# Performance work log

Measured on AMD Instinct MI355X. Metric: run time of the kernel, lower is better.

The kernel has to match this reference:

```python
import jax, jax.numpy as jnp
import numpy as np

B, N = 64, 196
D1, D2, H = 512, 2048, 512


def setup_inputs() -> dict:
    key = jax.random.key(0)
    ks = jax.random.split(key, 8)
    s1 = 1.0 / np.sqrt(D1)
    s2 = 1.0 / np.sqrt(D2)
    sh = 1.0 / np.sqrt(H)
    return {
        "input1": jax.random.normal(ks[0], (B, D1), jnp.float32),
        "input2": jax.random.normal(ks[1], (B, N, D2), jnp.float32),
        "W1": jax.random.uniform(ks[2], (D1, H), jnp.float32, -s1, s1),
        "b1": jax.random.uniform(ks[3], (H,), jnp.float32, -s1, s1),
        "W2": jax.random.uniform(ks[4], (D2, H), jnp.float32, -s2, s2),
        "b2": jax.random.uniform(ks[5], (H,), jnp.float32, -s2, s2),
        "Wf": jax.random.uniform(ks[6], (H, 1), jnp.float32, -sh, sh),
        "bf": jax.random.uniform(ks[7], (1,), jnp.float32, -sh, sh),
    }


def reference(input1, input2, W1, b1, W2, b2, Wf, bf):
    # enc1: [B, H]; enc2: [B, N, H]
    enc1 = input1 @ W1 + b1
    enc2 = jnp.einsum("bnd,dh->bnh", input2, W2) + b2
    # additive (Bahdanau) score: relu(enc2 + enc1[:,None]) @ Wf -> [B, N]
    scores = (jax.nn.relu(enc2 + enc1[:, None, :]) @ Wf)[..., 0] + bf[0]
    alpha = jax.nn.softmax(scores, axis=1)  # softmax over N regions
    att = jnp.einsum("bnd,bn->bd", input2, alpha)  # weighted sum of raw features
    return att, alpha
```

## Files before the change

kernel.cpp:

```cpp
#include <hip/hip_runtime.h>
#include <hip/hip_bf16.h>
#include <stdint.h>

#define BB 64
#define NN 196
#define D1c 512
#define D2c 2048
#define HHc 512
#define MM (BB*NN)

typedef __attribute__((ext_vector_type(8))) short bf16x8;
typedef __attribute__((ext_vector_type(4))) float f32x4;

__device__ inline ushort f2bf(float f){
  uint32_t u = __float_as_uint(f);
  u += 0x7fff + ((u >> 16) & 1);
  return (ushort)(u >> 16);
}
__device__ inline uint32_t cvtpk(float lo, float hi){
  uint32_t r;
  asm("v_cvt_pk_bf16_f32 %0, %1, %2" : "=v"(r) : "v"(lo), "v"(hi));
  return r;
}

__global__ __launch_bounds__(256) void w2t_kernel(const float* __restrict__ W2,
                                                  ushort* __restrict__ w2t){
  __shared__ float tile[64][65];
  const int kt = blockIdx.x;
  const int ht = blockIdx.y;
  const int t = threadIdx.x;
  const int tr = t >> 4;
  const int tc = (t & 15) * 4;
  #pragma unroll
  for (int p = 0; p < 4; ++p){
    int k = p*16 + tr;
    float4 v = *(const float4*)(W2 + (size_t)(kt*64 + k)*HHc + ht*64 + tc);
    tile[k][tc] = v.x; tile[k][tc+1] = v.y; tile[k][tc+2] = v.z; tile[k][tc+3] = v.w;
  }
  __syncthreads();
  #pragma unroll
  for (int p = 0; p < 4; ++p){
    int h = p*16 + tr;
    ushort4 o;
    o.x = f2bf(tile[tc  ][h]);
    o.y = f2bf(tile[tc+1][h]);
    o.z = f2bf(tile[tc+2][h]);
    o.w = f2bf(tile[tc+3][h]);
    *(ushort4*)(w2t + (size_t)(ht*64 + h)*D2c + kt*64 + tc) = o;
  }
}

__global__ __launch_bounds__(128) void enc1_kernel(const float* __restrict__ in1,
                                                   const float* __restrict__ W1,
                                                   const float* __restrict__ b1,
                                                   float* __restrict__ enc1){
  __shared__ float s1[D1c];
  const int b = blockIdx.x;
  const int ht = blockIdx.y;
  const int t = threadIdx.x;
  ((float4*)s1)[t] = ((const float4*)(in1 + (size_t)b*D1c))[t];
  __syncthreads();
  const int h = ht*128 + t;
  float acc = b1[h];
  #pragma unroll 8
  for (int d = 0; d < D1c; ++d)
    acc += s1[d] * W1[(size_t)d*HHc + h];
  enc1[b*HHc + h] = acc;
}

__global__ __launch_bounds__(512,2) void score_gemm(
    const float*  __restrict__ in2,
    const ushort* __restrict__ w2t,
    const float*  __restrict__ b2,
    const float*  __restrict__ wf,
    const float*  __restrict__ enc1,
    float*        __restrict__ scores)
{
  __shared__ ushort As[2][128*64];
  __shared__ ushort Bs[3][256*64];

  const int t = threadIdx.x;
  const int p   = blockIdx.x;
  const int xcd = p & 7;
  const int lg  = (xcd < 4 ? xcd*25 : 100 + (xcd-4)*24) + (p >> 3);
  const int h0  = (lg & 1) * 256;
  const int m0  = (lg >> 1) * 128;

  const int wave = t >> 6, lane = t & 63;
  const int wm = wave >> 2, whh = wave & 3;
  const int l15 = lane & 15, l4 = lane >> 4;

  const int rA = wave*16 + l4;
  const float* aBase = in2 + (size_t)(m0 + rA)*D2c + l15*4;
  const int acw  = l15 >> 1;
  const int apar = (l15 & 1) * 4;

  const int bl_r = lane >> 3;
  const int bl_c = (lane & 7) ^ bl_r;

  f32x4 acc[4][4];
  #pragma unroll
  for (int i = 0; i < 4; ++i)
    #pragma unroll
    for (int j = 0; j < 4; ++j) acc[i][j] = (f32x4)0.f;

  float4 aReg[4];

#define A_LOAD(kt)                                                           \
  { _Pragma("unroll")                                                        \
    for (int j = 0; j < 4; ++j)                                              \
      aReg[j] = *(const float4*)(aBase + (size_t)(j*4)*D2c + (kt)*64); }

#define A_WRITE(buf)                                                         \
  { _Pragma("unroll")                                                        \
    for (int j = 0; j < 4; ++j){                                             \
      int r = rA + j*4;                                                      \
      uint2 pk;                                                              \
      pk.x = cvtpk(aReg[j].x, aReg[j].y);                                    \
      pk.y = cvtpk(aReg[j].z, aReg[j].w);                                    \
      *(uint2*)(As[buf] + r*64 + ((acw ^ (r & 7)) << 3) + apar) = pk; } }

#define B_GLDS(kt, buf)                                                      \
  { _Pragma("unroll")                                                        \
    for (int i = 0; i < 4; ++i){                                             \
      int g = wave*4 + i;                                                    \
      const ushort* src = w2t + (size_t)(h0 + g*8 + bl_r)*D2c                \
                          + (kt)*64 + bl_c*8;                                \
      __builtin_amdgcn_global_load_lds(                                      \
          (const __attribute__((address_space(1))) uint32_t*)src,            \
          (__attribute__((address_space(3))) uint32_t*)(Bs[buf] + g*512),    \
          16, 0, 0); } }

#define COMPUTE(abuf, bbuf)                                                  \
  { _Pragma("unroll")                                                        \
    for (int kk = 0; kk < 2; ++kk){                                          \
      bf16x8 af[4], bfr[4];                                                  \
      _Pragma("unroll")                                                      \
      for (int mf = 0; mf < 4; ++mf){                                        \
        int r = wm*64 + mf*16 + l15, c = kk*4 + l4;                          \
        af[mf] = *(const bf16x8*)(As[abuf] + r*64 + ((c ^ (r & 7)) << 3)); } \
      _Pragma("unroll")                                                      \
      for (int hf = 0; hf < 4; ++hf){                                        \
        int r = whh*64 + hf*16 + l15, c = kk*4 + l4;                         \
        bfr[hf] = *(const bf16x8*)(Bs[bbuf] + r*64 + ((c ^ (r & 7)) << 3)); }\
      _Pragma("unroll")                                                      \
      for (int mf = 0; mf < 4; ++mf)                                         \
        _Pragma("unroll")                                                    \
        for (int hf = 0; hf < 4; ++hf)                                       \
          acc[mf][hf] = __builtin_amdgcn_mfma_f32_16x16x32_bf16(             \
              af[mf], bfr[hf], acc[mf][hf], 0, 0, 0); } }

#define SB0()    __builtin_amdgcn_sched_barrier(0)
#define WAITV(n) { asm volatile("s_waitcnt vmcnt(" #n ")" ::: "memory"); SB0(); }
#define LGKM0()  { asm volatile("s_waitcnt lgkmcnt(0)" ::: "memory"); SB0(); }
#define BAR()    { SB0(); __builtin_amdgcn_s_barrier(); SB0(); }

  A_LOAD(0);
  B_GLDS(0, 0);
  B_GLDS(1, 1);
  SB0();
  WAITV(8);
  A_WRITE(0);
  WAITV(4);
  LGKM0();
  BAR();

  #pragma unroll 1
  for (int kt = 0; kt < 30; ++kt){
    A_LOAD(kt + 1);
    B_GLDS(kt + 2, (kt + 2) % 3);
    SB0();
    COMPUTE(kt & 1, kt % 3);
    WAITV(4);
    A_WRITE((kt + 1) & 1);
    LGKM0();
    BAR();
  }
  A_LOAD(31);
  SB0();
  COMPUTE(0, 0);
  WAITV(0);
  A_WRITE(1);
  LGKM0();
  BAR();
  COMPUTE(1, 1);

  float b2v[4], wfv[4];
  #pragma unroll
  for (int hf = 0; hf < 4; ++hf){
    int hc = h0 + whh*64 + hf*16 + l15;
    b2v[hf] = b2[hc]; wfv[hf] = wf[hc];
  }
  #pragma unroll
  for (int mf = 0; mf < 4; ++mf){
    #pragma unroll
    for (int r = 0; r < 4; ++r){
      int m = m0 + wm*64 + mf*16 + l4*4 + r;
      int b = m / NN;
      const float* e1 = enc1 + (size_t)b*HHc + h0 + whh*64 + l15;
      float s = 0.f;
      #pragma unroll
      for (int hf = 0; hf < 4; ++hf){
        float v = acc[mf][hf][r] + b2v[hf] + e1[hf*16];
        s += fmaxf(v, 0.f) * wfv[hf];
      }
      s += __shfl_xor(s, 1); s += __shfl_xor(s, 2);
      s += __shfl_xor(s, 4); s += __shfl_xor(s, 8);
      if (l15 == 0) atomicAdd(&scores[m], s);
    }
  }
#undef A_LOAD
#undef A_WRITE
#undef B_GLDS
#undef COMPUTE
#undef WAITV
#undef LGKM0
#undef SB0
#undef BAR
}

__global__ __launch_bounds__(64) void softmax_kernel(const float* __restrict__ scores,
                                                     float* __restrict__ alpha){
  const int b = blockIdx.x, t = threadIdx.x;
  const float* s = scores + b*NN;
  float x[4]; float mx = -1e30f;
  #pragma unroll
  for (int i = 0; i < 4; ++i){
    int n = t + i*64;
    x[i] = (n < NN) ? s[n] : -1e30f;
    mx = fmaxf(mx, x[i]);
  }
  #pragma unroll
  for (int o = 1; o < 64; o <<= 1) mx = fmaxf(mx, __shfl_xor(mx, o));
  float sum = 0.f;
  #pragma unroll
  for (int i = 0; i < 4; ++i){
    int n = t + i*64;
    float e = (n < NN) ? __expf(x[i] - mx) : 0.f;
    x[i] = e; sum += e;
  }
  #pragma unroll
  for (int o = 1; o < 64; o <<= 1) sum += __shfl_xor(sum, o);
  float inv = 1.f / sum;
  #pragma unroll
  for (int i = 0; i < 4; ++i){
    int n = t + i*64;
    if (n < NN) alpha[b*NN + n] = x[i] * inv;
  }
}

__global__ __launch_bounds__(256) void att_kernel(const float* __restrict__ in2,
                                                  const float* __restrict__ alpha,
                                                  float* __restrict__ att){
  __shared__ float sal[NN];
  const int b = blockIdx.y;
  const int t = threadIdx.x;
  if (t < NN) sal[t] = alpha[b*NN + t];
  __syncthreads();
  const int d = blockIdx.x*256 + t;
  const float* src = in2 + (size_t)b*NN*D2c + d;
  float acc = 0.f;
  #pragma unroll 7
  for (int n = 0; n < NN; ++n)
    acc += src[(size_t)n*D2c] * sal[n];
  att[(size_t)b*D2c + d] = acc;
}

extern "C" void kernel_launch(void* const* d_in, const int* in_sizes, int n_in,
                              void* d_out, int out_size, void* d_ws, size_t ws_size,
                              hipStream_t stream){
  (void)in_sizes; (void)n_in; (void)out_size; (void)ws_size;
  const float* input1 = (const float*)d_in[0];
  const float* input2 = (const float*)d_in[1];
  const float* W1     = (const float*)d_in[2];
  const float* b1     = (const float*)d_in[3];
  const float* W2     = (const float*)d_in[4];
  const float* b2     = (const float*)d_in[5];
  const float* Wf     = (const float*)d_in[6];

  float* out   = (float*)d_out;
  float* att   = out;
  float* alpha = out + BB*D2c;

  char*   ws     = (char*)d_ws;
  ushort* w2t    = (ushort*)ws;
  float*  enc1   = (float*)(ws + 2*1024*1024);
  float*  scores = (float*)(ws + 2*1024*1024 + 131072);

  hipMemsetAsync(scores, 0, MM*sizeof(float), stream);
  w2t_kernel<<<dim3(32, 8), 256, 0, stream>>>(W2, w2t);
  enc1_kernel<<<dim3(BB, 4), 128, 0, stream>>>(input1, W1, b1, enc1);
  score_gemm<<<dim3(196), 512, 0, stream>>>(input2, w2t, b2, Wf, enc1, scores);
  softmax_kernel<<<dim3(BB), 64, 0, stream>>>(scores, alpha);
  att_kernel<<<dim3(8, BB), 256, 0, stream>>>(input2, alpha, att);
}
```

Before: 109.6 us.

## Double-buffer A register prefetch and interleave fragment reads with MFMA in GEMM loop

The fp32 A-tile global loads are now issued two k-steps ahead into alternating register sets, which gives them a full iteration of latency hiding. Both k-halves' LDS fragments are read up front, and partial lgkmcnt waits let the first MFMA batch start while later reads are still in flight. MFMA sections are wrapped in s_setprio to favour matrix issue. The cost is more registers (two A register sets, two fragment sets), which could lower occupancy or cause spills.

New measurement: 118.3 us. 1.08x slower.

```diff
diff --git a/kernel.cpp b/kernel.cpp
--- a/kernel.cpp
+++ b/kernel.cpp
@@ -104,20 +104,21 @@
     #pragma unroll
     for (int j = 0; j < 4; ++j) acc[i][j] = (f32x4)0.f;
 
-  float4 aReg[4];
-
-#define A_LOAD(kt)                                                           \
+  float4 aRegA[4], aRegB[4];
+  bf16x8 af0[4], bf0[4], af1[4], bf1[4];
+
+#define A_LOAD(kt, R)                                                        \
   { _Pragma("unroll")                                                        \
     for (int j = 0; j < 4; ++j)                                              \
-      aReg[j] = *(const float4*)(aBase + (size_t)(j*4)*D2c + (kt)*64); }
-
-#define A_WRITE(buf)                                                         \
+      R[j] = *(const float4*)(aBase + (size_t)(j*4)*D2c + (kt)*64); }
+
+#define A_WRITE(R, buf)                                                      \
   { _Pragma("unroll")                                                        \
     for (int j = 0; j < 4; ++j){                                             \
       int r = rA + j*4;                                                      \
       uint2 pk;                                                              \
-      pk.x = cvtpk(aReg[j].x, aReg[j].y);                                    \
-      pk.y = cvtpk(aReg[j].z, aReg[j].w);                                    \
+      pk.x = cvtpk(R[j].x, R[j].y);                                          \
+      pk.y = cvtpk(R[j].z, R[j].w);                                          \
       *(uint2*)(As[buf] + r*64 + ((acw ^ (r & 7)) << 3) + apar) = pk; } }
 
 #define B_GLDS(kt, buf)                                                      \
@@ -131,59 +132,92 @@
           (__attribute__((address_space(3))) uint32_t*)(Bs[buf] + g*512),    \
           16, 0, 0); } }
 
-#define COMPUTE(abuf, bbuf)                                                  \
+#define READ_FRAGS(abuf, bbuf, kk, AF, BF)                                   \
   { _Pragma("unroll")                                                        \
-    for (int kk = 0; kk < 2; ++kk){                                          \
-      bf16x8 af[4], bfr[4];                                                  \
+    for (int mf = 0; mf < 4; ++mf){                                          \
+      int r = wm*64 + mf*16 + l15, c = (kk)*4 + l4;                          \
+      AF[mf] = *(const bf16x8*)(As[abuf] + r*64 + ((c ^ (r & 7)) << 3)); }   \
+    _Pragma("unroll")                                                        \
+    for (int hf = 0; hf < 4; ++hf){                                          \
+      int r = whh*64 + hf*16 + l15, c = (kk)*4 + l4;                         \
+      BF[hf] = *(const bf16x8*)(Bs[bbuf] + r*64 + ((c ^ (r & 7)) << 3)); } }
+
+#define MFMA16(AF, BF)                                                       \
+  { __builtin_amdgcn_s_setprio(1);                                           \
+    _Pragma("unroll")                                                        \
+    for (int mf = 0; mf < 4; ++mf)                                           \
       _Pragma("unroll")                                                      \
-      for (int mf = 0; mf < 4; ++mf){                                        \
-        int r = wm*64 + mf*16 + l15, c = kk*4 + l4;                          \
-        af[mf] = *(const bf16x8*)(As[abuf] + r*64 + ((c ^ (r & 7)) << 3)); } \
-      _Pragma("unroll")                                                      \
-      for (int hf = 0; hf < 4; ++hf){                                        \
-        int r = whh*64 + hf*16 + l15, c = kk*4 + l4;                         \
-        bfr[hf] = *(const bf16x8*)(Bs[bbuf] + r*64 + ((c ^ (r & 7)) << 3)); }\
-      _Pragma("unroll")                                                      \
-      for (int mf = 0; mf < 4; ++mf)                                         \
-        _Pragma("unroll")                                                    \
-        for (int hf = 0; hf < 4; ++hf)                                       \
-          acc[mf][hf] = __builtin_amdgcn_mfma_f32_16x16x32_bf16(             \
-              af[mf], bfr[hf], acc[mf][hf], 0, 0, 0); } }
+      for (int hf = 0; hf < 4; ++hf)                                         \
+        acc[mf][hf] = __builtin_amdgcn_mfma_f32_16x16x32_bf16(               \
+            AF[mf], BF[hf], acc[mf][hf], 0, 0, 0);                           \
+    __builtin_amdgcn_s_setprio(0); }
 
 #define SB0()    __builtin_amdgcn_sched_barrier(0)
 #define WAITV(n) { asm volatile("s_waitcnt vmcnt(" #n ")" ::: "memory"); SB0(); }
-#define LGKM0()  { asm volatile("s_waitcnt lgkmcnt(0)" ::: "memory"); SB0(); }
+#define LGKM(n)  { asm volatile("s_waitcnt lgkmcnt(" #n ")" ::: "memory"); SB0(); }
 #define BAR()    { SB0(); __builtin_amdgcn_s_barrier(); SB0(); }
 
-  A_LOAD(0);
+  A_LOAD(0, aRegA);
+  SB0();
   B_GLDS(0, 0);
   B_GLDS(1, 1);
   SB0();
+  A_LOAD(1, aRegB);
+  SB0();
+  WAITV(12);
+  A_WRITE(aRegA, 0);
   WAITV(8);
-  A_WRITE(0);
-  WAITV(4);
-  LGKM0();
+  LGKM(0);
   BAR();
 
   #pragma unroll 1
   for (int kt = 0; kt < 30; ++kt){
-    A_LOAD(kt + 1);
+    const int ab = kt & 1;
+    const int bb = kt % 3;
+    READ_FRAGS(ab, bb, 0, af0, bf0);
+    SB0();
     B_GLDS(kt + 2, (kt + 2) % 3);
     SB0();
-    COMPUTE(kt & 1, kt % 3);
-    WAITV(4);
-    A_WRITE((kt + 1) & 1);
-    LGKM0();
+    READ_FRAGS(ab, bb, 1, af1, bf1);
+    SB0();
+    LGKM(8);
+    MFMA16(af0, bf0);
+    if (ab == 0){ A_LOAD(kt + 2, aRegA); } else { A_LOAD(kt + 2, aRegB); }
+    SB0();
+    WAITV(8);
+    if (ab == 0){ A_WRITE(aRegB, 1); } else { A_WRITE(aRegA, 0); }
+    SB0();
+    LGKM(4);
+    MFMA16(af1, bf1);
+    LGKM(0);
     BAR();
   }
-  A_LOAD(31);
-  SB0();
-  COMPUTE(0, 0);
-  WAITV(0);
-  A_WRITE(1);
-  LGKM0();
-  BAR();
-  COMPUTE(1, 1);
+
+  {
+    READ_FRAGS(0, 0, 0, af0, bf0);
+    SB0();
+    READ_FRAGS(0, 0, 1, af1, bf1);
+    SB0();
+    LGKM(8);
+    MFMA16(af0, bf0);
+    WAITV(0);
+    A_WRITE(aRegB, 1);
+    SB0();
+    LGKM(4);
+    MFMA16(af1, bf1);
+    LGKM(0);
+    BAR();
+  }
+  {
+    READ_FRAGS(1, 1, 0, af0, bf0);
+    SB0();
+    READ_FRAGS(1, 1, 1, af1, bf1);
+    SB0();
+    LGKM(8);
+    MFMA16(af0, bf0);
+    LGKM(0);
+    MFMA16(af1, bf1);
+  }
 
   float b2v[4], wfv[4];
   #pragma unroll
@@ -212,9 +246,10 @@
 #undef A_LOAD
 #undef A_WRITE
 #undef B_GLDS
-#undef COMPUTE
+#undef READ_FRAGS
+#undef MFMA16
 #undef WAITV
-#undef LGKM0
+#undef LGKM
 #undef SB0
 #undef BAR
 }
```
